# Kernel optimization log

Hardware: AMD Instinct MI355X
Metric: run time of the kernel (lower is better)

## Reference

```python
import jax, jax.numpy as jnp
import numpy as np

N = 100000      # nodes
R = 3           # relations
E = 1600000     # edges per relation
IN, HID, OUT = 128, 128, 64


def setup_inputs() -> dict:
    key = jax.random.key(0)
    ks = jax.random.split(key, 16)
    x = jax.random.normal(ks[0], (N, IN), dtype=jnp.float32)
    src = jax.random.randint(ks[1], (R, E), 0, N, dtype=jnp.int32)
    dst = jax.random.randint(ks[2], (R, E), 0, N, dtype=jnp.int32)
    dims = [(IN, HID), (HID, HID), (HID, HID), (HID, HID), (HID, HID), (HID, OUT)]
    inp = {"x": x, "src": src, "dst": dst}
    for i, (di, do) in enumerate(dims):
        w = jax.random.normal(ks[3 + i], (R, di, do), dtype=jnp.float32) / np.sqrt(di).astype(np.float32)
        inp[f"W{i+1}"] = w
        inp[f"b{i+1}"] = jnp.zeros((R, do), dtype=jnp.float32)
    return inp


def _degree_norms(src, dst):
    # GraphConv norm='both': scale by out-deg(src)^-1/2 before, in-deg(dst)^-1/2 after
    ones = jnp.ones((E,), dtype=jnp.float32)
    inv_out, inv_in = [], []
    for r in range(R):
        d_out = jax.ops.segment_sum(ones, src[r], num_segments=N)
        d_in = jax.ops.segment_sum(ones, dst[r], num_segments=N)
        inv_out.append(jax.lax.rsqrt(jnp.maximum(d_out, 1.0))[:, None])
        inv_in.append(jax.lax.rsqrt(jnp.maximum(d_in, 1.0))[:, None])
    return inv_out, inv_in


def _hetero_conv(h, W, b, src, dst, inv_out, inv_in):
    # sum over relations of GraphConv_r(h): D_dst^-1/2 A_r (D_src^-1/2 h) W_r + b_r
    out = None
    for r in range(R):
        m = (h * inv_out[r]) @ W[r]                      # [N, do], weight-first (same math)
        agg = jax.ops.segment_sum(m[src[r]], dst[r], num_segments=N)
        term = agg * inv_in[r] + b[r]
        out = term if out is None else out + term
    return out


def reference(x, src, dst, W1, b1, W2, b2, W3, b3, W4, b4, W5, b5, W6, b6):
    inv_out, inv_in = _degree_norms(src, dst)
    h = x
    for W, b in [(W1, b1), (W2, b2), (W3, b3), (W4, b4), (W5, b5)]:
        h = jax.nn.relu(_hetero_conv(h, W, b, src, dst, inv_out, inv_in))
    return _hetero_conv(h, W6, b6, src, dst, inv_out, inv_in)
```

## Files before the change

kernel.cpp:

```cpp
#include <hip/hip_runtime.h>
#include <hip/hip_bf16.h>
#include <hip/hip_fp16.h>

constexpr int N_NODES = 100000;
constexpr int N_REL   = 3;
constexpr int N_EDGE  = 1600000;
constexpr int NCHUNK  = (N_NODES + 1023) / 1024;

constexpr int CCHUNK = 50;
constexpr int CH     = N_EDGE / CCHUNK;
constexpr int SUBN   = 50000;
constexpr int WPP    = SUBN / 4;
constexpr int CWORDS = N_NODES / 4;

constexpr int BSH  = 7;
constexpr int BNPB = 1 << BSH;
constexpr int NB   = (N_NODES + BNPB - 1) / BNPB;

typedef __attribute__((ext_vector_type(8))) short short8;
typedef __attribute__((ext_vector_type(4))) float f32x4;

__device__ inline ushort f2bf(float x) {
  unsigned u = __float_as_uint(x);
  unsigned r = u + 0x7FFFu + ((u >> 16) & 1u);
  return (ushort)(r >> 16);
}
__device__ inline float bf2f(ushort h) { return __uint_as_float(((unsigned)h) << 16); }


__global__ __launch_bounds__(1024)
void count_kernel(const int* __restrict__ src, const int* __restrict__ dst,
                  uint* __restrict__ part) {
  int c = blockIdx.x, r = blockIdx.y, dir = blockIdx.z;
  const int* ids = (dir ? dst : src) + (size_t)r * N_EDGE + (size_t)c * CH;
  uint* p = part + ((size_t)(c * N_REL + r) * 2 + dir) * CWORDS;
  __shared__ uint hist[WPP];
  #pragma unroll
  for (int pass = 0; pass < 2; pass++) {
    int base = pass * SUBN;
    for (int i = threadIdx.x; i < WPP; i += 1024) hist[i] = 0u;
    __syncthreads();
    for (int e = (int)threadIdx.x; e < CH; e += 1024) {
      int ln = ids[e] - base;
      if ((unsigned)ln < (unsigned)SUBN)
        atomicAdd(&hist[ln >> 2], 1u << ((ln & 3) * 8));
    }
    __syncthreads();
    for (int i = threadIdx.x; i < WPP; i += 1024) p[pass * WPP + i] = hist[i];
    __syncthreads();
  }
}

__global__ void reduce_kernel(const uint* __restrict__ part,
                              int* __restrict__ deg_out, int* __restrict__ deg_in) {
  int i = blockIdx.x * 256 + threadIdx.x;
  if (i >= N_REL * CWORDS) return;
  int r = i / CWORDS, w = i % CWORDS;
  uint aoe = 0, aoo = 0, aie = 0, aio = 0;
  for (int c = 0; c < CCHUNK; c++) {
    uint vo = part[((size_t)(c * N_REL + r) * 2 + 0) * CWORDS + w];
    uint vi = part[((size_t)(c * N_REL + r) * 2 + 1) * CWORDS + w];
    aoe += vo & 0x00FF00FFu; aoo += (vo >> 8) & 0x00FF00FFu;
    aie += vi & 0x00FF00FFu; aio += (vi >> 8) & 0x00FF00FFu;
  }
  int4 dout = make_int4((int)(aoe & 0xFFFFu), (int)(aoo & 0xFFFFu),
                        (int)(aoe >> 16),     (int)(aoo >> 16));
  int4 din  = make_int4((int)(aie & 0xFFFFu), (int)(aio & 0xFFFFu),
                        (int)(aie >> 16),     (int)(aio >> 16));
  *(int4*)&deg_out[(size_t)r * N_NODES + w * 4] = dout;
  *(int4*)&deg_in [(size_t)r * N_NODES + w * 4] = din;
}

__global__ void inv_kernel(const int* __restrict__ deg_out, const int* __restrict__ deg_in,
                           float* __restrict__ inv_out, float* __restrict__ inv_in) {
  int i = blockIdx.x * blockDim.x + threadIdx.x;
  if (i >= N_REL * N_NODES) return;
  inv_out[i] = rsqrtf(fmaxf((float)deg_out[i], 1.0f));
  inv_in[i]  = rsqrtf(fmaxf((float)deg_in[i],  1.0f));
}

__global__ void scan1_kernel(const int* __restrict__ deg_in, int* __restrict__ excl,
                             int* __restrict__ part) {
  int r = blockIdx.y;
  int i = blockIdx.x * 1024 + threadIdx.x;
  int v = (i < N_NODES) ? deg_in[r * N_NODES + i] : 0;
  __shared__ int sm[1024];
  sm[threadIdx.x] = v;
  __syncthreads();
  for (int off = 1; off < 1024; off <<= 1) {
    int t = (threadIdx.x >= (unsigned)off) ? sm[threadIdx.x - off] : 0;
    __syncthreads();
    sm[threadIdx.x] += t;
    __syncthreads();
  }
  if (i < N_NODES) excl[r * N_NODES + i] = sm[threadIdx.x] - v;
  if (threadIdx.x == 1023) part[r * NCHUNK + blockIdx.x] = sm[1023];
}

__global__ void scan2_kernel(int* __restrict__ part) {
  int r = blockIdx.x;
  int* p = part + r * NCHUNK;
  __shared__ int sm[128];
  int tid = threadIdx.x;
  int v = (tid < NCHUNK) ? p[tid] : 0;
  sm[tid] = v;
  __syncthreads();
  for (int off = 1; off < 128; off <<= 1) {
    int t = (tid >= off) ? sm[tid - off] : 0;
    __syncthreads();
    sm[tid] += t;
    __syncthreads();
  }
  if (tid < NCHUNK) p[tid] = sm[tid] - v;
}

__global__ void scan3_kernel(const int* __restrict__ excl, const int* __restrict__ part,
                             int* __restrict__ row_off) {
  int r = blockIdx.y;
  int i = blockIdx.x * 1024 + threadIdx.x;
  if (i < N_NODES) row_off[r * (N_NODES + 1) + i] = excl[r * N_NODES + i] + part[r * NCHUNK + (i >> 10)];
  if (i == N_NODES) row_off[r * (N_NODES + 1) + N_NODES] = N_EDGE;
}


__global__ __launch_bounds__(64)
void boff_kernel(const uint* __restrict__ cpart, int* __restrict__ boff) {
  int b = blockIdx.x, r = blockIdx.y;
  int lane = threadIdx.x;
  __shared__ int cnt_l[CCHUNK];
  for (int c = 0; c < CCHUNK; c++) {
    int w = b * 32 + (lane & 31);
    uint v = 0;
    if (w < CWORDS)
      v = cpart[((size_t)(c * N_REL + r) * 2 + 1) * CWORDS + w];
    int s = (int)((v & 0xFFu) + ((v >> 8) & 0xFFu) + ((v >> 16) & 0xFFu) + (v >> 24));
    #pragma unroll
    for (int k = 16; k >= 1; k >>= 1) s += __shfl_xor(s, k);
    if (lane == 0) cnt_l[c] = s;
  }
  __syncthreads();
  if (lane == 0) {
    int run = 0;
    for (int c = 0; c < CCHUNK; c++) { int t = cnt_l[c]; cnt_l[c] = run; run += t; }
  }
  __syncthreads();
  for (int c = lane; c < CCHUNK; c += 64)
    boff[((size_t)c * N_REL + r) * NB + b] = cnt_l[c];
}

__global__ __launch_bounds__(1024)
void bin2_kernel(const int* __restrict__ src, const int* __restrict__ dst,
                 const int* __restrict__ row_off, const int* __restrict__ boff,
                 int2* __restrict__ binned) {
  int c = blockIdx.x, r = blockIdx.y;
  __shared__ int cur[NB];
  for (int j = threadIdx.x; j < NB; j += 1024)
    cur[j] = row_off[r * (N_NODES + 1) + (j << BSH)] + boff[((size_t)c * N_REL + r) * NB + j];
  __syncthreads();
  const int* sp = src + (size_t)r * N_EDGE + (size_t)c * CH;
  const int* dp = dst + (size_t)r * N_EDGE + (size_t)c * CH;
  int2* bp = binned + (size_t)r * N_EDGE;
  for (int e = (int)threadIdx.x; e < CH; e += 1024) {
    int s = sp[e], d = dp[e];
    int slot = atomicAdd(&cur[d >> BSH], 1);
    bp[slot] = make_int2(s, d);
  }
}

__global__ __launch_bounds__(256)
void scatter2_kernel(const int2* __restrict__ binned, const int* __restrict__ row_off,
                     const float* __restrict__ inv_out, const float* __restrict__ inv_in,
                     float2* __restrict__ sorted_sc) {
  int b = blockIdx.x, r = blockIdx.y;
  int node0 = b << BSH;
  int node1 = min(node0 + BNPB, N_NODES);
  const int* ro = row_off + r * (N_NODES + 1);
  int base = ro[node0];
  int m    = ro[node1] - base;
  __shared__ int cur[BNPB];
  for (int j = threadIdx.x; j < node1 - node0; j += 256)
    cur[j] = ro[node0 + j] - base;
  __syncthreads();
  const int2* bp = binned + (size_t)r * N_EDGE + base;
  float2* op = sorted_sc + (size_t)r * N_EDGE + base;
  const float* ivo = inv_out + r * N_NODES;
  const float* ivi = inv_in  + r * N_NODES;
  for (int i = threadIdx.x; i < m; i += 256) {
    int2 rec = bp[i];
    int pos = atomicAdd(&cur[rec.y - node0], 1);
    float coef = ivo[rec.x] * ivi[rec.y];
    op[pos] = make_float2(__int_as_float(rec.x), coef);
  }
}

__global__ void convw_kernel(const float* __restrict__ W, ushort* __restrict__ Wh,
                             ushort* __restrict__ Wl, int DOv) {
  int idx = blockIdx.x * 256 + threadIdx.x;
  if (idx >= 384 * DOv) return;
  int k = idx / DOv, c = idx % DOv;
  float v = W[idx];
  ushort hh = f2bf(v);
  Wh[c * 384 + k] = hh;
  Wl[c * 384 + k] = f2bf(v - bf2f(hh));
}

__global__ void convx_kernel(const float* __restrict__ x, ushort* __restrict__ x16) {
  int i = blockIdx.x * 256 + threadIdx.x;
  if (i >= N_NODES * 32) return;
  f32x4 v = ((const f32x4*)x)[i];
  __half2 h0 = __floats2half2_rn(v.x, v.y);
  __half2 h1 = __floats2half2_rn(v.z, v.w);
  uint2 o;
  o.x = *(const unsigned*)&h0;
  o.y = *(const unsigned*)&h1;
  ((uint2*)x16)[i] = o;
}


template<int P>
__device__ inline void agg_pairs(const float2* __restrict__ scp, const uint2* __restrict__ hp,
                                 int e, int sub, int l32, f32x4& acc) {
  float2 q[P];
  #pragma unroll
  for (int j = 0; j < P; j++) q[j] = scp[e + 2 * j + sub];
  uint2 v[P];
  #pragma unroll
  for (int j = 0; j < P; j++) v[j] = hp[(size_t)__float_as_int(q[j].x) * 32 + l32];
  #pragma unroll
  for (int j = 0; j < P; j++) {
    __half2 h0 = *(const __half2*)&v[j].x;
    __half2 h1 = *(const __half2*)&v[j].y;
    float2 f0 = __half22float2(h0);
    float2 f1 = __half22float2(h1);
    acc.x = fmaf(q[j].y, f0.x, acc.x);
    acc.y = fmaf(q[j].y, f0.y, acc.y);
    acc.z = fmaf(q[j].y, f1.x, acc.z);
    acc.w = fmaf(q[j].y, f1.y, acc.w);
  }
}

__launch_bounds__(256)
__global__ void agg_kernel(const ushort* __restrict__ h, const float2* __restrict__ sc,
                           const int* __restrict__ row_off,
                           ushort* __restrict__ agg16) {
  int r    = blockIdx.y;
  int node = blockIdx.x * 4 + ((int)threadIdx.x >> 6);
  int lane = (int)threadIdx.x & 63;
  int sub  = lane >> 5;
  int l32  = lane & 31;
  if (node >= N_NODES) return;
  const int* ro = row_off + r * (N_NODES + 1);
  int beg = ro[node], end = ro[node + 1];
  const float2* scp = sc + (size_t)r * N_EDGE;
  const uint2* hp = (const uint2*)h;
  f32x4 acc = (f32x4){0.f, 0.f, 0.f, 0.f};
  int e = beg;
  while (e + 16 <= end) { agg_pairs<8>(scp, hp, e, sub, l32, acc); e += 16; }
  if (e + 8 <= end)     { agg_pairs<4>(scp, hp, e, sub, l32, acc); e += 8; }
  if (e + 4 <= end)     { agg_pairs<2>(scp, hp, e, sub, l32, acc); e += 4; }
  if (e + 2 <= end)     { agg_pairs<1>(scp, hp, e, sub, l32, acc); e += 2; }
  if (e < end && sub == 0) {
    float2 q = scp[e];
    uint2 v = hp[(size_t)__float_as_int(q.x) * 32 + l32];
    __half2 h0 = *(const __half2*)&v.x;
    __half2 h1 = *(const __half2*)&v.y;
    float2 f0 = __half22float2(h0);
    float2 f1 = __half22float2(h1);
    acc.x = fmaf(q.y, f0.x, acc.x);
    acc.y = fmaf(q.y, f0.y, acc.y);
    acc.z = fmaf(q.y, f1.x, acc.z);
    acc.w = fmaf(q.y, f1.y, acc.w);
  }
  acc.x += __shfl_xor(acc.x, 32);
  acc.y += __shfl_xor(acc.y, 32);
  acc.z += __shfl_xor(acc.z, 32);
  acc.w += __shfl_xor(acc.w, 32);
  float a0 = (sub == 0) ? acc.x : acc.z;
  float a1 = (sub == 0) ? acc.y : acc.w;
  __half2 hv = __floats2half2_rn(a0, a1);
  size_t base = (size_t)node * 384 + r * 128 + l32 * 4 + sub * 2;
  *(unsigned*)(agg16 + base) = *(const unsigned*)&hv;
}

template<int DO, bool F16OUT>
__launch_bounds__(256)
__global__ void gemm_kernel(const ushort* __restrict__ A16,
                            const ushort* __restrict__ Wh, const ushort* __restrict__ Wl,
                            const float* __restrict__ b, float* __restrict__ out,
                            ushort* __restrict__ out16, int apply_relu) {
  constexpr int K   = 384;
  constexpr int KC  = 32;
  constexpr int NCT = DO / 16;
  constexpr int LDA = 40;
  __shared__ ushort As_hi[128 * LDA], As_lo[128 * LDA];
  __shared__ ushort Bs_hi[DO * LDA],  Bs_lo[DO * LDA];
  int tid  = threadIdx.x;
  int wave = tid >> 6, lane = tid & 63;
  int quad = lane >> 4, m16 = lane & 15;
  int m0 = blockIdx.x * 128;

  f32x4 acc[2][NCT];
  #pragma unroll
  for (int rt = 0; rt < 2; rt++)
    #pragma unroll
    for (int ct = 0; ct < NCT; ct++) acc[rt][ct] = (f32x4){0.f, 0.f, 0.f, 0.f};

  for (int kc = 0; kc < K; kc += KC) {
    __syncthreads();
    #pragma unroll
    for (int it = 0; it < 2; it++) {
      int idx = it * 256 + tid;
      int row = idx >> 2, kq = (idx & 3) * 8;
      uint4 vh = make_uint4(0u, 0u, 0u, 0u), vl = make_uint4(0u, 0u, 0u, 0u);
      if (m0 + row < N_NODES) {
        uint4 va = *(const uint4*)(A16 + (size_t)(m0 + row) * K + kc + kq);
        const ushort* hs = (const ushort*)&va;
        ushort* hh = (ushort*)&vh;
        ushort* ll = (ushort*)&vl;
        #pragma unroll
        for (int j = 0; j < 8; j++) {
          float f = __half2float(*(const __half*)&hs[j]);
          ushort hi = f2bf(f);
          hh[j] = hi;
          ll[j] = f2bf(f - bf2f(hi));
        }
      }
      *(uint4*)&As_hi[row * LDA + kq] = vh;
      *(uint4*)&As_lo[row * LDA + kq] = vl;
    }
    #pragma unroll
    for (int it = 0; it < DO / 64; it++) {
      int idx = it * 256 + tid;
      int n = idx >> 2, kq = (idx & 3) * 8;
      *(uint4*)&Bs_hi[n * LDA + kq] = *(const uint4*)(Wh + (size_t)n * K + kc + kq);
      *(uint4*)&Bs_lo[n * LDA + kq] = *(const uint4*)(Wl + (size_t)n * K + kc + kq);
    }
    __syncthreads();

    short8 ah[2], al[2];
    #pragma unroll
    for (int rt = 0; rt < 2; rt++) {
      int m = wave * 32 + rt * 16 + m16;
      ah[rt] = *(const short8*)&As_hi[m * LDA + quad * 8];
      al[rt] = *(const short8*)&As_lo[m * LDA + quad * 8];
    }
    #pragma unroll
    for (int ct = 0; ct < NCT; ct++) {
      int n = ct * 16 + m16;
      short8 bh = *(const short8*)&Bs_hi[n * LDA + quad * 8];
      short8 bl = *(const short8*)&Bs_lo[n * LDA + quad * 8];
      #pragma unroll
      for (int rt = 0; rt < 2; rt++) {
        acc[rt][ct] = __builtin_amdgcn_mfma_f32_16x16x32_bf16(ah[rt], bh, acc[rt][ct], 0, 0, 0);
        acc[rt][ct] = __builtin_amdgcn_mfma_f32_16x16x32_bf16(ah[rt], bl, acc[rt][ct], 0, 0, 0);
        acc[rt][ct] = __builtin_amdgcn_mfma_f32_16x16x32_bf16(al[rt], bh, acc[rt][ct], 0, 0, 0);
      }
    }
  }
  #pragma unroll
  for (int ct = 0; ct < NCT; ct++) {
    int col = ct * 16 + m16;
    float bs = b[col] + b[DO + col] + b[2 * DO + col];
    #pragma unroll
    for (int rt = 0; rt < 2; rt++) {
      #pragma unroll
      for (int v = 0; v < 4; v++) {
        int row = m0 + wave * 32 + rt * 16 + quad * 4 + v;
        if (row < N_NODES) {
          float o = acc[rt][ct][v] + bs;
          if (apply_relu) o = fmaxf(o, 0.f);
          if (F16OUT) {
            __half ho = __float2half_rn(o);
            out16[(size_t)row * DO + col] = *(const ushort*)&ho;
          } else {
            out[(size_t)row * DO + col] = o;
          }
        }
      }
    }
  }
}


extern "C" void kernel_launch(void* const* d_in, const int* in_sizes, int n_in,
                              void* d_out, int out_size, void* d_ws, size_t ws_size,
                              hipStream_t stream) {
  const float* x   = (const float*)d_in[0];
  const int*   src = (const int*)d_in[1];
  const int*   dst = (const int*)d_in[2];
  const float* Wl6[6]; const float* bl[6];
  for (int i = 0; i < 6; i++) { Wl6[i] = (const float*)d_in[3 + 2*i]; bl[i] = (const float*)d_in[4 + 2*i]; }

  char* ws = (char*)d_ws;
  size_t off = 0;
  auto take = [&](size_t bytes) -> char* {
    char* p = ws + off;
    off = (off + bytes + 255) & ~(size_t)255;
    return p;
  };
  ushort* h16     = (ushort*)take((size_t)N_NODES * 128 * 2);
  ushort* agg16   = (ushort*)take((size_t)N_NODES * 384 * 2);
  int*    deg     = (int*)  take((size_t)2 * N_REL * N_NODES * 4);
  int*    deg_out = deg;
  int*    deg_in  = deg + N_REL * N_NODES;
  float*  inv_out = (float*)take((size_t)N_REL * N_NODES * 4);
  float*  inv_in  = (float*)take((size_t)N_REL * N_NODES * 4);
  int*    row_off = (int*)  take((size_t)N_REL * (N_NODES + 1) * 4);
  int*    part    = (int*)  take((size_t)N_REL * NCHUNK * 4);
  int*    boff    = (int*)  take((size_t)CCHUNK * N_REL * NB * 4);
  float2* s_sc    = (float2*)take((size_t)N_REL * N_EDGE * 8);
  ushort* Wt      = (ushort*)take((size_t)6 * 384 * 128 * 2 * 2);
  int*    excl    = (int*)agg16;
  int2*   binned  = (int2*)((char*)agg16 + (size_t)(2 << 20));
  uint*   cpart   = (uint*)((char*)agg16 + (size_t)(41 << 20));
  (void)ws_size; (void)in_sizes; (void)n_in; (void)out_size;

  const int nblocks = (N_REL * N_NODES + 255) / 256;

  count_kernel<<<dim3(CCHUNK, N_REL, 2), 1024, 0, stream>>>(src, dst, cpart);
  reduce_kernel<<<(N_REL * CWORDS + 255) / 256, 256, 0, stream>>>(cpart, deg_out, deg_in);
  inv_kernel<<<nblocks, 256, 0, stream>>>(deg_out, deg_in, inv_out, inv_in);
  scan1_kernel<<<dim3(NCHUNK, 3), 1024, 0, stream>>>(deg_in, excl, part);
  scan2_kernel<<<3, 128, 0, stream>>>(part);
  scan3_kernel<<<dim3(NCHUNK + 1, 3), 1024, 0, stream>>>(excl, part, row_off);
  boff_kernel<<<dim3(NB, N_REL), 64, 0, stream>>>(cpart, boff);
  bin2_kernel<<<dim3(CCHUNK, N_REL), 1024, 0, stream>>>(src, dst, row_off, boff, binned);
  scatter2_kernel<<<dim3(NB, N_REL), 256, 0, stream>>>(binned, row_off, inv_out, inv_in, s_sc);

  convx_kernel<<<(N_NODES * 32 + 255) / 256, 256, 0, stream>>>(x, h16);

  ushort* Wh[6]; ushort* Wlo[6];
  {
    size_t woff = 0;
    for (int L = 0; L < 6; L++) {
      int DOv = (L < 5) ? 128 : 64;
      Wh[L]  = Wt + woff;  woff += (size_t)384 * DOv;
      Wlo[L] = Wt + woff;  woff += (size_t)384 * DOv;
      convw_kernel<<<(384 * DOv + 255) / 256, 256, 0, stream>>>(Wl6[L], Wh[L], Wlo[L], DOv);
    }
  }

  const int mtiles = (N_NODES + 127) / 128;
  const int agg_blocks = (N_NODES + 3) / 4;
  for (int L = 0; L < 6; L++) {
    agg_kernel<<<dim3(agg_blocks, 3), 256, 0, stream>>>(h16, s_sc, row_off, agg16);
    if (L < 5) {
      gemm_kernel<128, true><<<mtiles, 256, 0, stream>>>(agg16, Wh[L], Wlo[L], bl[L],
                                                         nullptr, h16, 1);
    } else {
      gemm_kernel<64, false><<<mtiles, 256, 0, stream>>>(agg16, Wh[L], Wlo[L], bl[L],
                                                         (float*)d_out, nullptr, 0);
    }
  }
}
```

Before: 1.739 ms.

## Pack edge records into 32-bit words with 17-bit source and fp16 coefficient

Binned edges are stored as one 32-bit word holding the source index and the destination's low bits, replacing an int2. Sorted edges hold the 17-bit source and a 15-bit fp16 coefficient with the sign bit dropped, replacing a float2. This halves the edge-record traffic in bin, scatter and the six aggregation passes, at the cost of rounding the coefficient to fp16 and relying on node ids fitting in 17 bits.

```diff
diff --git a/kernel.cpp b/kernel.cpp
--- a/kernel.cpp
+++ b/kernel.cpp
@@ -151,7 +151,7 @@
 __global__ __launch_bounds__(1024)
 void bin2_kernel(const int* __restrict__ src, const int* __restrict__ dst,
                  const int* __restrict__ row_off, const int* __restrict__ boff,
-                 int2* __restrict__ binned) {
+                 uint* __restrict__ binned) {
   int c = blockIdx.x, r = blockIdx.y;
   __shared__ int cur[NB];
   for (int j = threadIdx.x; j < NB; j += 1024)
@@ -159,18 +159,18 @@
   __syncthreads();
   const int* sp = src + (size_t)r * N_EDGE + (size_t)c * CH;
   const int* dp = dst + (size_t)r * N_EDGE + (size_t)c * CH;
-  int2* bp = binned + (size_t)r * N_EDGE;
+  uint* bp = binned + (size_t)r * N_EDGE;
   for (int e = (int)threadIdx.x; e < CH; e += 1024) {
     int s = sp[e], d = dp[e];
     int slot = atomicAdd(&cur[d >> BSH], 1);
-    bp[slot] = make_int2(s, d);
+    bp[slot] = ((uint)(d & (BNPB - 1)) << 17) | (uint)s;
   }
 }
 
 __global__ __launch_bounds__(256)
-void scatter2_kernel(const int2* __restrict__ binned, const int* __restrict__ row_off,
+void scatter2_kernel(const uint* __restrict__ binned, const int* __restrict__ row_off,
                      const float* __restrict__ inv_out, const float* __restrict__ inv_in,
-                     float2* __restrict__ sorted_sc) {
+                     uint* __restrict__ sorted_sc) {
   int b = blockIdx.x, r = blockIdx.y;
   int node0 = b << BSH;
   int node1 = min(node0 + BNPB, N_NODES);
@@ -181,15 +181,20 @@
   for (int j = threadIdx.x; j < node1 - node0; j += 256)
     cur[j] = ro[node0 + j] - base;
   __syncthreads();
-  const int2* bp = binned + (size_t)r * N_EDGE + base;
-  float2* op = sorted_sc + (size_t)r * N_EDGE + base;
+  const uint* bp = binned + (size_t)r * N_EDGE + base;
+  uint* op = sorted_sc + (size_t)r * N_EDGE + base;
   const float* ivo = inv_out + r * N_NODES;
   const float* ivi = inv_in  + r * N_NODES;
   for (int i = threadIdx.x; i < m; i += 256) {
-    int2 rec = bp[i];
-    int pos = atomicAdd(&cur[rec.y - node0], 1);
-    float coef = ivo[rec.x] * ivi[rec.y];
-    op[pos] = make_float2(__int_as_float(rec.x), coef);
+    uint rec = bp[i];
+    int s    = (int)(rec & 0x1FFFFu);
+    int dlow = (int)((rec >> 17) & (uint)(BNPB - 1));
+    int d    = node0 + dlow;
+    int pos  = atomicAdd(&cur[dlow], 1);
+    float coef = ivo[s] * ivi[d];
+    __half ch = __float2half_rn(coef);
+    uint cb = (uint)(*(const ushort*)&ch) & 0x7FFFu;
+    op[pos] = (cb << 17) | (uint)s;
   }
 }
 
@@ -218,29 +223,31 @@
 
 
 template<int P>
-__device__ inline void agg_pairs(const float2* __restrict__ scp, const uint2* __restrict__ hp,
+__device__ inline void agg_pairs(const uint* __restrict__ scp, const uint2* __restrict__ hp,
                                  int e, int sub, int l32, f32x4& acc) {
-  float2 q[P];
+  uint q[P];
   #pragma unroll
   for (int j = 0; j < P; j++) q[j] = scp[e + 2 * j + sub];
   uint2 v[P];
   #pragma unroll
-  for (int j = 0; j < P; j++) v[j] = hp[(size_t)__float_as_int(q[j].x) * 32 + l32];
+  for (int j = 0; j < P; j++) v[j] = hp[(size_t)(q[j] & 0x1FFFFu) * 32 + l32];
   #pragma unroll
   for (int j = 0; j < P; j++) {
+    ushort cb = (ushort)(q[j] >> 17);
+    float cf = __half2float(*(const __half*)&cb);
     __half2 h0 = *(const __half2*)&v[j].x;
     __half2 h1 = *(const __half2*)&v[j].y;
     float2 f0 = __half22float2(h0);
     float2 f1 = __half22float2(h1);
-    acc.x = fmaf(q[j].y, f0.x, acc.x);
-    acc.y = fmaf(q[j].y, f0.y, acc.y);
-    acc.z = fmaf(q[j].y, f1.x, acc.z);
-    acc.w = fmaf(q[j].y, f1.y, acc.w);
+    acc.x = fmaf(cf, f0.x, acc.x);
+    acc.y = fmaf(cf, f0.y, acc.y);
+    acc.z = fmaf(cf, f1.x, acc.z);
+    acc.w = fmaf(cf, f1.y, acc.w);
   }
 }
 
 __launch_bounds__(256)
-__global__ void agg_kernel(const ushort* __restrict__ h, const float2* __restrict__ sc,
+__global__ void agg_kernel(const ushort* __restrict__ h, const uint* __restrict__ sc,
                            const int* __restrict__ row_off,
                            ushort* __restrict__ agg16) {
   int r    = blockIdx.y;
@@ -251,7 +258,7 @@
   if (node >= N_NODES) return;
   const int* ro = row_off + r * (N_NODES + 1);
   int beg = ro[node], end = ro[node + 1];
-  const float2* scp = sc + (size_t)r * N_EDGE;
+  const uint* scp = sc + (size_t)r * N_EDGE;
   const uint2* hp = (const uint2*)h;
   f32x4 acc = (f32x4){0.f, 0.f, 0.f, 0.f};
   int e = beg;
@@ -260,16 +267,18 @@
   if (e + 4 <= end)     { agg_pairs<2>(scp, hp, e, sub, l32, acc); e += 4; }
   if (e + 2 <= end)     { agg_pairs<1>(scp, hp, e, sub, l32, acc); e += 2; }
   if (e < end && sub == 0) {
-    float2 q = scp[e];
-    uint2 v = hp[(size_t)__float_as_int(q.x) * 32 + l32];
+    uint q = scp[e];
+    uint2 v = hp[(size_t)(q & 0x1FFFFu) * 32 + l32];
+    ushort cb = (ushort)(q >> 17);
+    float cf = __half2float(*(const __half*)&cb);
     __half2 h0 = *(const __half2*)&v.x;
     __half2 h1 = *(const __half2*)&v.y;
     float2 f0 = __half22float2(h0);
     float2 f1 = __half22float2(h1);
-    acc.x = fmaf(q.y, f0.x, acc.x);
-    acc.y = fmaf(q.y, f0.y, acc.y);
-    acc.z = fmaf(q.y, f1.x, acc.z);
-    acc.w = fmaf(q.y, f1.y, acc.w);
+    acc.x = fmaf(cf, f0.x, acc.x);
+    acc.y = fmaf(cf, f0.y, acc.y);
+    acc.z = fmaf(cf, f1.x, acc.z);
+    acc.w = fmaf(cf, f1.y, acc.w);
   }
   acc.x += __shfl_xor(acc.x, 32);
   acc.y += __shfl_xor(acc.y, 32);
@@ -408,11 +417,11 @@
   int*    row_off = (int*)  take((size_t)N_REL * (N_NODES + 1) * 4);
   int*    part    = (int*)  take((size_t)N_REL * NCHUNK * 4);
   int*    boff    = (int*)  take((size_t)CCHUNK * N_REL * NB * 4);
-  float2* s_sc    = (float2*)take((size_t)N_REL * N_EDGE * 8);
+  uint*   s_sc    = (uint*) take((size_t)N_REL * N_EDGE * 4);
   ushort* Wt      = (ushort*)take((size_t)6 * 384 * 128 * 2 * 2);
   int*    excl    = (int*)agg16;
-  int2*   binned  = (int2*)((char*)agg16 + (size_t)(2 << 20));
-  uint*   cpart   = (uint*)((char*)agg16 + (size_t)(41 << 20));
+  uint*   binned  = (uint*)((char*)agg16 + (size_t)(2 << 20));
+  uint*   cpart   = (uint*)((char*)agg16 + (size_t)(22 << 20));
   (void)ws_size; (void)in_sizes; (void)n_in; (void)out_size;
 
   const int nblocks = (N_REL * N_NODES + 255) / 256;
```

Measured after the change: 1.663 ms. 1.05x faster.
